# Kernel tuning notes

Hardware: AMD Instinct MI355X
Metric: run time of the kernel (lower is better)

Reference implementation:

```python
import jax, jax.numpy as jnp
import numpy as np

N_NODES = 50000
N_EDGES = 1_000_000
D = 256


def gcn_conv(x, src, dst, ew, W, b, n):
    # PyG GCNConv with edge_weight: linear transform, add self-loops (w=1),
    # symmetric normalization deg^{-1/2} w deg^{-1/2}, scatter-sum, + bias.
    x = x @ W  # (n, out)
    loop = jnp.arange(n)
    src_l = jnp.concatenate([src, loop])
    dst_l = jnp.concatenate([dst, loop])
    ew_l = jnp.concatenate([ew, jnp.ones((n,), ew.dtype)])
    deg = jax.ops.segment_sum(ew_l, dst_l, num_segments=n)
    dinv = jnp.where(deg > 0, jax.lax.rsqrt(deg), 0.0).astype(x.dtype)
    norm = dinv[src_l] * ew_l * dinv[dst_l]  # (E+n,)
    out = jax.ops.segment_sum(norm[:, None] * x[src_l], dst_l, num_segments=n)
    return out + b


def setup_inputs() -> dict:
    key = jax.random.key(0)
    k = jax.random.split(key, 8)
    glorot = 1.0 / np.sqrt(D)
    return {
        "x": jax.random.normal(k[0], (N_NODES, D), jnp.float32),
        "edge_index": jax.random.randint(k[1], (2, N_EDGES), 0, N_NODES, jnp.int64),
        "edge_weight": jax.random.uniform(k[2], (N_EDGES,), jnp.float32),
        "W1": jax.random.normal(k[3], (D, D), jnp.float32) * glorot,
        "b1": jnp.zeros((D,), jnp.float32),
        "W2": jax.random.normal(k[4], (D, D), jnp.float32) * glorot,
        "b2": jnp.zeros((D,), jnp.float32),
    }


def reference(x, edge_index, edge_weight, W1, b1, W2, b2):
    n = x.shape[0]
    src, dst = edge_index[0], edge_index[1]
    h = gcn_conv(x, src, dst, edge_weight, W1, b1, n)
    h = jax.nn.relu(h)  # dropout is identity at eval
    out = gcn_conv(h, src, dst, edge_weight, W2, b2, n)
    return out
```

## Files before the change

### kernel.cpp

```cpp
#include <hip/hip_runtime.h>
#include <hip/hip_bf16.h>
#include <stdint.h>


#define D 256
#define CAP 64

typedef __attribute__((ext_vector_type(8))) short short8;
typedef __attribute__((ext_vector_type(4))) float floatx4;

__device__ inline unsigned short f2bf_rne(float f) {
    union { float f; uint32_t u; } v; v.f = f;
    uint32_t u = v.u;
    return (unsigned short)((u + 0x7FFFu + ((u >> 16) & 1u)) >> 16);
}
__device__ inline float bf_lo(uint32_t u) { union { uint32_t u; float f; } v; v.u = u << 16; return v.f; }
__device__ inline float bf_hi(uint32_t u) { union { uint32_t u; float f; } v; v.u = u & 0xFFFF0000u; return v.f; }

#define FXS 16777216.0f

#define GBM 128
#define GBN 128
#define GBK 32
#define LDA 40
#define NB_CVT 64
#define NB_P1 1600
#define EPL 136

__device__ inline void epilogue_store(floatx4 (&acc)[4][4], unsigned short* __restrict__ C,
                                      unsigned char* smem, int n, int bm, int bn,
                                      int t, int w, int lq, int lr, int wn) {
    unsigned short* lds16 = (unsigned short*)smem;
    #pragma unroll
    for (int h = 0; h < 2; h++) {
        __syncthreads();
        if ((w >> 1) == h) {
            #pragma unroll
            for (int i = 0; i < 4; i++)
                #pragma unroll
                for (int j = 0; j < 4; j++)
                    #pragma unroll
                    for (int r = 0; r < 4; r++)
                        lds16[(i * 16 + lq * 4 + r) * EPL + wn + j * 16 + lr] =
                            f2bf_rne(acc[i][j][r]);
        }
        __syncthreads();
        #pragma unroll
        for (int it = 0; it < 4; it++) {
            int idx = t + it * 256;
            int row = idx >> 4;
            int ch = idx & 15;
            int grow = bm + h * 64 + row;
            if (grow < n)
                *(uint4*)&C[(size_t)grow * D + bn + ch * 8] =
                    *(const uint4*)&lds16[row * EPL + ch * 8];
        }
    }
}

__device__ void gemm1_block(const float* __restrict__ x, const float* __restrict__ W1,
                            unsigned short* __restrict__ C, int n, int bid,
                            unsigned char* smem) {
    unsigned short (*As)[LDA] = (unsigned short(*)[LDA])smem;
    unsigned short (*Bs)[LDA] = (unsigned short(*)[LDA])(smem + GBM * LDA * 2);
    int t = threadIdx.x;
    int bm = (bid >> 1) * GBM;
    int bn = (bid & 1) * GBN;
    int w = t >> 6, l = t & 63;
    int wm = (w >> 1) * 64, wn = (w & 1) * 64;
    int lr = l & 15;
    int lq = l >> 4;
    floatx4 acc[4][4] = {};
    for (int k0 = 0; k0 < D; k0 += GBK) {
        #pragma unroll
        for (int i = 0; i < 2; i++) {
            int c = t + i * 256;
            int row = c >> 2;
            int kk = (c & 3) * 8;
            int gr = bm + row;
            short8 av = {};
            if (gr < n) {
                const float* ap = x + (size_t)gr * D + k0 + kk;
                float4 f0 = *(const float4*)ap;
                float4 f1 = *(const float4*)(ap + 4);
                av[0] = (short)f2bf_rne(f0.x); av[1] = (short)f2bf_rne(f0.y);
                av[2] = (short)f2bf_rne(f0.z); av[3] = (short)f2bf_rne(f0.w);
                av[4] = (short)f2bf_rne(f1.x); av[5] = (short)f2bf_rne(f1.y);
                av[6] = (short)f2bf_rne(f1.z); av[7] = (short)f2bf_rne(f1.w);
            }
            *(short8*)&As[row][kk] = av;
        }
        #pragma unroll
        for (int i = 0; i < 4; i++) {
            int idx = t + i * 256;
            int kk = idx >> 5;
            int nn4 = (idx & 31) << 2;
            float4 wv = *(const float4*)(W1 + (size_t)(k0 + kk) * D + bn + nn4);
            Bs[nn4 + 0][kk] = f2bf_rne(wv.x);
            Bs[nn4 + 1][kk] = f2bf_rne(wv.y);
            Bs[nn4 + 2][kk] = f2bf_rne(wv.z);
            Bs[nn4 + 3][kk] = f2bf_rne(wv.w);
        }
        __syncthreads();
        short8 af[4], bfr[4];
        #pragma unroll
        for (int i = 0; i < 4; i++) af[i] = *(const short8*)&As[wm + i * 16 + lr][lq * 8];
        #pragma unroll
        for (int j = 0; j < 4; j++) bfr[j] = *(const short8*)&Bs[wn + j * 16 + lr][lq * 8];
        #pragma unroll
        for (int i = 0; i < 4; i++)
            #pragma unroll
            for (int j = 0; j < 4; j++)
                acc[i][j] = __builtin_amdgcn_mfma_f32_16x16x32_bf16(af[i], bfr[j], acc[i][j], 0, 0, 0);
        __syncthreads();
    }
    epilogue_store(acc, C, smem, n, bm, bn, t, w, lq, lr, wn);
}

__device__ void cvtw2_block(const float* __restrict__ W2, unsigned short* __restrict__ Wt,
                            int bid, unsigned char* smem) {
    float (*sw)[33] = (float(*)[33])smem;
    int k0 = (bid >> 3) * 32, n0 = (bid & 7) * 32;
    int t = threadIdx.x;
    int tx = t & 31, ty0 = (t >> 5) * 4;
    #pragma unroll
    for (int r = 0; r < 4; r++)
        sw[ty0 + r][tx] = W2[(size_t)(k0 + ty0 + r) * D + n0 + tx];
    __syncthreads();
    #pragma unroll
    for (int r = 0; r < 4; r++)
        Wt[(size_t)(n0 + ty0 + r) * D + k0 + tx] = f2bf_rne(sw[tx][ty0 + r]);
}

__device__ void pass1_block(const int* __restrict__ src, const int* __restrict__ dst,
                            const float* __restrict__ ew,
                            unsigned long long* __restrict__ packed,
                            unsigned long long* __restrict__ edata, int E, int bid, int nb) {
    int stride = nb * 256;
    for (int e = bid * 256 + threadIdx.x; e < E; e += stride) {
        int d = __builtin_nontemporal_load(&dst[e]);
        float w = __builtin_nontemporal_load(&ew[e]);
        uint32_t fx = __float2uint_rn(w * FXS);
        unsigned long long old =
            atomicAdd(&packed[(size_t)d << 3], ((unsigned long long)fx << 32) | 1ull);
        uint32_t r = (uint32_t)old;
        if (r < CAP) {
            int s = __builtin_nontemporal_load(&src[e]);
            unsigned long long pv =
                ((unsigned long long)__float_as_uint(w) << 32) | (uint32_t)s;
            edata[((size_t)d << 6) + r] = pv;
        }
    }
}

__global__ __launch_bounds__(256) void fused1_kernel(const float* __restrict__ x,
                                                     const float* __restrict__ W1,
                                                     const float* __restrict__ W2,
                                                     const int* __restrict__ src,
                                                     const int* __restrict__ dst,
                                                     const float* __restrict__ ew,
                                                     unsigned short* __restrict__ xws,
                                                     unsigned short* __restrict__ w2t,
                                                     unsigned long long* __restrict__ packed,
                                                     unsigned long long* __restrict__ edata,
                                                     int n, int E, int nb_gemm) {
    __shared__ unsigned char smem[2 * GBM * LDA * 2];
    int bid = blockIdx.x;
    if (bid < nb_gemm) {
        gemm1_block(x, W1, xws, n, bid, smem);
    } else if (bid < nb_gemm + NB_CVT) {
        cvtw2_block(W2, w2t, bid - nb_gemm, smem);
    } else {
        pass1_block(src, dst, ew, packed, edata, E, bid - nb_gemm - NB_CVT, NB_P1);
    }
}

__global__ void unpack_kernel(const unsigned long long* __restrict__ packed,
                              float* __restrict__ dinv, int n) {
    int i = blockIdx.x * 256 + threadIdx.x;
    if (i < n) {
        float deg = (float)(packed[(size_t)i << 3] >> 32) * (1.0f / FXS) + 1.0f;
        dinv[i] = rsqrtf(deg);
    }
}

__global__ __launch_bounds__(256) void gemm2_kernel(const unsigned short* __restrict__ A,
                                                    const unsigned short* __restrict__ Bt,
                                                    unsigned short* __restrict__ C, int n) {
    __shared__ unsigned short As[64][LDA];
    __shared__ unsigned short Bs[GBN][LDA];
    int t = threadIdx.x;
    int bm = blockIdx.x * 64;
    int bn = blockIdx.y * GBN;
    int w = t >> 6, l = t & 63;
    int wm = (w >> 1) * 32, wn = (w & 1) * 64;
    int lr = l & 15;
    int lq = l >> 4;
    floatx4 acc[2][4] = {};
    for (int k0 = 0; k0 < D; k0 += GBK) {
        {
            int row = t >> 2;
            int kk = (t & 3) * 8;
            int gr = bm + row;
            short8 av = {};
            if (gr < n) av = *(const short8*)&A[(size_t)gr * D + k0 + kk];
            *(short8*)&As[row][kk] = av;
        }
        #pragma unroll
        for (int i = 0; i < 2; i++) {
            int c = t + i * 256;
            int row = c >> 2;
            int kk = (c & 3) * 8;
            short8 bv = *(const short8*)&Bt[(size_t)(bn + row) * D + k0 + kk];
            *(short8*)&Bs[row][kk] = bv;
        }
        __syncthreads();
        short8 af[2], bfr[4];
        #pragma unroll
        for (int i = 0; i < 2; i++) af[i] = *(const short8*)&As[wm + i * 16 + lr][lq * 8];
        #pragma unroll
        for (int j = 0; j < 4; j++) bfr[j] = *(const short8*)&Bs[wn + j * 16 + lr][lq * 8];
        #pragma unroll
        for (int i = 0; i < 2; i++)
            #pragma unroll
            for (int j = 0; j < 4; j++)
                acc[i][j] = __builtin_amdgcn_mfma_f32_16x16x32_bf16(af[i], bfr[j], acc[i][j], 0, 0, 0);
        __syncthreads();
    }
    #pragma unroll
    for (int i = 0; i < 2; i++) {
        #pragma unroll
        for (int r = 0; r < 4; r++) {
            int row = bm + wm + i * 16 + lq * 4 + r;
            if (row >= n) continue;
            #pragma unroll
            for (int j = 0; j < 4; j++) {
                int col = bn + wn + j * 16 + lr;
                C[(size_t)row * D + col] = f2bf_rne(acc[i][j][r]);
            }
        }
    }
}

template <bool RELU, bool OUT_BF16>
__global__ __launch_bounds__(256) void gather_kernel(const unsigned short* __restrict__ xw,
                                                     const uint2* __restrict__ edata,
                                                     const unsigned long long* __restrict__ packed,
                                                     const float* __restrict__ dinv,
                                                     const float* __restrict__ bias,
                                                     void* __restrict__ outv, int n) {
    int wid = threadIdx.x >> 6;
    int lane = threadIdx.x & 63;
    int node = (blockIdx.x << 2) + wid;
    if (node >= n) return;
    int half = lane >> 5;
    int cl = lane & 31;
    int ch = cl << 3;
    float di = dinv[node];

    float acc[8];
    {
        uint4 r = *(const uint4*)(xw + (size_t)node * D + ch);
        float4 b0 = *(const float4*)(bias + ch);
        float4 b1 = *(const float4*)(bias + ch + 4);
        float ws = (half == 0) ? di * di : 0.0f;
        float bs = (half == 0) ? 1.0f : 0.0f;
        acc[0] = ws * bf_lo(r.x) + bs * b0.x;
        acc[1] = ws * bf_hi(r.x) + bs * b0.y;
        acc[2] = ws * bf_lo(r.y) + bs * b0.z;
        acc[3] = ws * bf_hi(r.y) + bs * b0.w;
        acc[4] = ws * bf_lo(r.z) + bs * b1.x;
        acc[5] = ws * bf_hi(r.z) + bs * b1.y;
        acc[6] = ws * bf_lo(r.w) + bs * b1.z;
        acc[7] = ws * bf_hi(r.w) + bs * b1.w;
    }

    int cnt = (int)(uint32_t)packed[(size_t)node << 3];
    cnt = min(cnt, CAP);
    const uint2* ebase = edata + ((size_t)node << 6);

    for (int j = 0; j < cnt; j += 8) {
        #pragma unroll
        for (int k = 0; k < 4; k++) {
            int e = j + 2 * k + half;
            bool valid = e < cnt;
            uint2 m; m.x = (uint32_t)node; m.y = 0u;
            if (valid) m = ebase[e];
            float co = dinv[m.x] * __uint_as_float(m.y) * di;
            uint4 r = *(const uint4*)(xw + (size_t)m.x * D + ch);
            acc[0] += co * bf_lo(r.x);
            acc[1] += co * bf_hi(r.x);
            acc[2] += co * bf_lo(r.y);
            acc[3] += co * bf_hi(r.y);
            acc[4] += co * bf_lo(r.z);
            acc[5] += co * bf_hi(r.z);
            acc[6] += co * bf_lo(r.w);
            acc[7] += co * bf_hi(r.w);
        }
    }
    #pragma unroll
    for (int k = 0; k < 8; k++) acc[k] += __shfl_xor(acc[k], 32);

    if (RELU) {
        #pragma unroll
        for (int k = 0; k < 8; k++) acc[k] = fmaxf(acc[k], 0.0f);
    }
    if (OUT_BF16) {
        if (half == 0) {
            uint4 o;
            o.x = (uint32_t)f2bf_rne(acc[0]) | ((uint32_t)f2bf_rne(acc[1]) << 16);
            o.y = (uint32_t)f2bf_rne(acc[2]) | ((uint32_t)f2bf_rne(acc[3]) << 16);
            o.z = (uint32_t)f2bf_rne(acc[4]) | ((uint32_t)f2bf_rne(acc[5]) << 16);
            o.w = (uint32_t)f2bf_rne(acc[6]) | ((uint32_t)f2bf_rne(acc[7]) << 16);
            *(uint4*)((unsigned short*)outv + (size_t)node * D + ch) = o;
        }
    } else {
        floatx4 o;
        int b = half * 4;
        o[0] = acc[b + 0]; o[1] = acc[b + 1]; o[2] = acc[b + 2]; o[3] = acc[b + 3];
        __builtin_nontemporal_store(o, (floatx4*)((float*)outv + (size_t)node * D + ch + b));
    }
}

extern "C" void kernel_launch(void* const* d_in, const int* in_sizes, int n_in,
                              void* d_out, int out_size, void* d_ws, size_t ws_size,
                              hipStream_t stream) {
    const float* x  = (const float*)d_in[0];
    const int*   ei = (const int*)d_in[1];
    const float* ew = (const float*)d_in[2];
    const float* W1 = (const float*)d_in[3];
    const float* b1 = (const float*)d_in[4];
    const float* W2 = (const float*)d_in[5];
    const float* b2 = (const float*)d_in[6];
    float* out = (float*)d_out;

    const int n = in_sizes[0] / D;
    const int E = in_sizes[2];
    const int* src = ei;
    const int* dst = ei + E;

    char* ws = (char*)d_ws;
    size_t off = 0;
    auto carve = [&](size_t bytes) {
        char* p = ws + off;
        off = (off + bytes + 255) & ~(size_t)255;
        return p;
    };
    unsigned long long* packed = (unsigned long long*)carve((size_t)n * 64);
    float*          dinv = (float*)carve((size_t)n * 4);
    unsigned long long* edata = (unsigned long long*)carve((size_t)n * CAP * 8);
    unsigned short* w2t  = (unsigned short*)carve((size_t)D * D * 2);
    unsigned short* xws  = (unsigned short*)carve((size_t)n * D * 2);
    unsigned short* hb   = (unsigned short*)carve((size_t)n * D * 2);

    const int nb_gemm = ((n + GBM - 1) / GBM) * 2;
    const int nb_node = (n + 255) / 256;

    (void)hipMemsetAsync(packed, 0, (size_t)n * 64, stream);

    fused1_kernel<<<nb_gemm + NB_CVT + NB_P1, 256, 0, stream>>>(
        x, W1, W2, src, dst, ew, xws, w2t, packed, edata, n, E, nb_gemm);

    unpack_kernel<<<nb_node, 256, 0, stream>>>(packed, dinv, n);

    dim3 agrid((n + 3) / 4);
    gather_kernel<true, true><<<agrid, 256, 0, stream>>>(xws, (const uint2*)edata, packed, dinv, b1, hb, n);

    dim3 ggrid((n + 63) / 64, D / GBN);
    gemm2_kernel<<<ggrid, 256, 0, stream>>>(hb, w2t, xws, n);

    gather_kernel<false, false><<<agrid, 256, 0, stream>>>(xws, (const uint2*)edata, packed, dinv, b2, out, n);
}
```

Measured before the change: 366.1 us.

## Pipeline layer-1 gather with GEMM2 over node chunks in fused launches

The layer-1 gather and the second GEMM are split into four node chunks and run as five fused launches. Each launch computes the gather for chunk k and the GEMM for chunk k-1, so the memory-bound gather and the compute-bound GEMM run concurrently. GEMM2 now writes to a separate buffer, xws2, because the gather blocks still read xws. This adds workspace and extra launches, and the smaller per-launch grids may leave tails underfilled.

After: 406.9 us. 1.11x slower.

```diff
diff --git a/kernel.cpp b/kernel.cpp
--- a/kernel.cpp
+++ b/kernel.cpp
@@ -184,14 +184,15 @@
     }
 }
 
-__global__ __launch_bounds__(256) void gemm2_kernel(const unsigned short* __restrict__ A,
-                                                    const unsigned short* __restrict__ Bt,
-                                                    unsigned short* __restrict__ C, int n) {
-    __shared__ unsigned short As[64][LDA];
-    __shared__ unsigned short Bs[GBN][LDA];
+__device__ void gemm2_block(const unsigned short* __restrict__ A,
+                            const unsigned short* __restrict__ Bt,
+                            unsigned short* __restrict__ C, int n,
+                            int bid, int tile0, unsigned char* smem) {
+    unsigned short (*As)[LDA] = (unsigned short(*)[LDA])smem;
+    unsigned short (*Bs)[LDA] = (unsigned short(*)[LDA])(smem + 64 * LDA * 2);
     int t = threadIdx.x;
-    int bm = blockIdx.x * 64;
-    int bn = blockIdx.y * GBN;
+    int bm = (tile0 + (bid >> 1)) * 64;
+    int bn = (bid & 1) * GBN;
     int w = t >> 6, l = t & 63;
     int wm = (w >> 1) * 32, wn = (w & 1) * 64;
     int lr = l & 15;
@@ -243,16 +244,16 @@
 }
 
 template <bool RELU, bool OUT_BF16>
-__global__ __launch_bounds__(256) void gather_kernel(const unsigned short* __restrict__ xw,
-                                                     const uint2* __restrict__ edata,
-                                                     const unsigned long long* __restrict__ packed,
-                                                     const float* __restrict__ dinv,
-                                                     const float* __restrict__ bias,
-                                                     void* __restrict__ outv, int n) {
+__device__ void gather_block(const unsigned short* __restrict__ xw,
+                             const uint2* __restrict__ edata,
+                             const unsigned long long* __restrict__ packed,
+                             const float* __restrict__ dinv,
+                             const float* __restrict__ bias,
+                             void* __restrict__ outv, int node_end, int node0, int bid) {
     int wid = threadIdx.x >> 6;
     int lane = threadIdx.x & 63;
-    int node = (blockIdx.x << 2) + wid;
-    if (node >= n) return;
+    int node = node0 + (bid << 2) + wid;
+    if (node >= node_end) return;
     int half = lane >> 5;
     int cl = lane & 31;
     int ch = cl << 3;
@@ -322,6 +323,36 @@
     }
 }
 
+__global__ __launch_bounds__(256) void fusedg_kernel(const unsigned short* __restrict__ hbA,
+                                                     const unsigned short* __restrict__ w2t,
+                                                     unsigned short* __restrict__ xws2,
+                                                     const unsigned short* __restrict__ xws,
+                                                     const uint2* __restrict__ edata,
+                                                     const unsigned long long* __restrict__ packed,
+                                                     const float* __restrict__ dinv,
+                                                     const float* __restrict__ b1,
+                                                     unsigned short* __restrict__ hbO,
+                                                     int n, int nbg, int tile0,
+                                                     int node0, int node_end) {
+    __shared__ unsigned char smem[(64 + GBN) * LDA * 2];
+    int bid = blockIdx.x;
+    if (bid < nbg) {
+        gemm2_block(hbA, w2t, xws2, n, bid, tile0, smem);
+    } else {
+        gather_block<true, true>(xws, edata, packed, dinv, b1, hbO,
+                                 node_end, node0, bid - nbg);
+    }
+}
+
+__global__ __launch_bounds__(256) void gather2_kernel(const unsigned short* __restrict__ xw,
+                                                      const uint2* __restrict__ edata,
+                                                      const unsigned long long* __restrict__ packed,
+                                                      const float* __restrict__ dinv,
+                                                      const float* __restrict__ bias,
+                                                      float* __restrict__ outv, int n) {
+    gather_block<false, false>(xw, edata, packed, dinv, bias, outv, n, 0, blockIdx.x);
+}
+
 extern "C" void kernel_launch(void* const* d_in, const int* in_sizes, int n_in,
                               void* d_out, int out_size, void* d_ws, size_t ws_size,
                               hipStream_t stream) {
@@ -351,6 +382,7 @@
     unsigned long long* edata = (unsigned long long*)carve((size_t)n * CAP * 8);
     unsigned short* w2t  = (unsigned short*)carve((size_t)D * D * 2);
     unsigned short* xws  = (unsigned short*)carve((size_t)n * D * 2);
+    unsigned short* xws2 = (unsigned short*)carve((size_t)n * D * 2);
     unsigned short* hb   = (unsigned short*)carve((size_t)n * D * 2);
 
     const int nb_gemm = ((n + GBM - 1) / GBM) * 2;
@@ -363,11 +395,31 @@
 
     unpack_kernel<<<nb_node, 256, 0, stream>>>(packed, dinv, n);
 
-    dim3 agrid((n + 3) / 4);
-    gather_kernel<true, true><<<agrid, 256, 0, stream>>>(xws, (const uint2*)edata, packed, dinv, b1, hb, n);
-
-    dim3 ggrid((n + 63) / 64, D / GBN);
-    gemm2_kernel<<<ggrid, 256, 0, stream>>>(hb, w2t, xws, n);
-
-    gather_kernel<false, false><<<agrid, 256, 0, stream>>>(xws, (const uint2*)edata, packed, dinv, b2, out, n);
-}
+    const int T64 = (n + 63) / 64;
+    const int cpt = (T64 + 3) / 4;
+    for (int ds = 0; ds < 5; ds++) {
+        int nbg = 0, gt0 = 0;
+        if (ds >= 1) {
+            gt0 = (ds - 1) * cpt;
+            int ngt = T64 - gt0;
+            if (ngt > cpt) ngt = cpt;
+            if (ngt < 0) ngt = 0;
+            nbg = ngt * 2;
+        }
+        int node0 = 0, node_end = 0, nba = 0;
+        if (ds < 4) {
+            node0 = ds * cpt * 64;
+            node_end = (ds + 1) * cpt * 64;
+            if (node_end > n) node_end = n;
+            if (node0 < node_end) nba = (node_end - node0 + 3) / 4;
+        }
+        int nb = nbg + nba;
+        if (nb == 0) continue;
+        fusedg_kernel<<<nb, 256, 0, stream>>>(hb, w2t, xws2, xws, (const uint2*)edata,
+                                              packed, dinv, b1, hb,
+                                              n, nbg, gt0, node0, node_end);
+    }
+
+    gather2_kernel<<<(n + 3) / 4, 256, 0, stream>>>(xws2, (const uint2*)edata,
+                                                    packed, dinv, b2, out, n);
+}
```
